# Kernel tuning notes

Measured on AMD Instinct MI355X. Metric: run time of the kernel, lower is better.

The kernel has to match this reference:

```python
import jax, jax.numpy as jnp
import numpy as np

B, S, D, H = 1, 4096, 1024, 16
DH = D // H

def setup_inputs() -> dict:
    key = jax.random.key(0)
    ks = jax.random.split(key, 5)
    std = float(np.sqrt(2.0 / (D + D)))
    return {
        "x": jax.random.normal(ks[0], (B, S, D), dtype=jnp.float32),
        "Wq": jax.random.normal(ks[1], (D, D), dtype=jnp.float32) * std,
        "Wk": jax.random.normal(ks[2], (D, D), dtype=jnp.float32) * std,
        "Wv": jax.random.normal(ks[3], (D, D), dtype=jnp.float32) * std,
        "Wo": jax.random.normal(ks[4], (D, D), dtype=jnp.float32) * std,
    }

def reference(x, Wq, Wk, Wv, Wo):
    # projections: input @ W.T, then split heads: b s (h d) -> b h s d
    def split_heads(t):
        b, s, _ = t.shape
        return t.reshape(b, s, H, DH).transpose(0, 2, 1, 3)
    q = split_heads(x @ Wq.T)
    k = split_heads(x @ Wk.T)
    v = split_heads(x @ Wv.T)
    scale = 1.0 / jnp.sqrt(jnp.asarray(DH, dtype=x.dtype))
    scores = jnp.einsum("bhqd,bhkd->bhqk", q, k) * scale  # (b,h,s,s)
    # causal mask: allow k <= q
    causal = jnp.tril(jnp.ones((S, S), dtype=bool))
    scores = jnp.where(causal, scores, jnp.finfo(scores.dtype).min)
    attn = jax.nn.softmax(scores, axis=-1)
    out = jnp.einsum("bhqk,bhkd->bhqd", attn, v)  # (b,h,s,d)
    out = out.transpose(0, 2, 1, 3).reshape(B, S, D)  # b h s d -> b s (h d)
    return out @ Wo.T
```

## Files before the change

### kernel.cpp

```cpp
#include <hip/hip_runtime.h>
#include <math.h>

#define SEQ 4096
#define DM  1024
#define NH  16
#define DH  64
#define NS  4

typedef _Float16 h16;
typedef __attribute__((ext_vector_type(4))) _Float16 h16x4;
typedef __attribute__((ext_vector_type(8))) _Float16 h16x8;
typedef __attribute__((ext_vector_type(4))) float f32x4;

__device__ __forceinline__ void gload_lds16(const h16* g, h16* l) {
    __builtin_amdgcn_global_load_lds(
        (const __attribute__((address_space(1))) void*)g,
        (__attribute__((address_space(3))) void*)l, 16, 0, 0);
}

__global__ __launch_bounds__(256) void cvt_all(const float* __restrict__ x,
                                               const float* __restrict__ wq,
                                               const float* __restrict__ wk,
                                               const float* __restrict__ wv,
                                               const float* __restrict__ wo,
                                               h16* __restrict__ dst) {
    const size_t SD4 = (size_t)SEQ * DM / 4;
    const size_t DD4 = (size_t)DM * DM / 4;
    const size_t i = (size_t)blockIdx.x * 256 + threadIdx.x;
    const float* src;
    size_t off;
    if (i < SD4) { src = x; off = i; }
    else {
        const size_t j = i - SD4;
        const int wsel = (int)(j >> 18);
        off = j & (DD4 - 1);
        src = (wsel == 0) ? wq : (wsel == 1) ? wk : (wsel == 2) ? wv : wo;
    }
    const float4 v = ((const float4*)src)[off];
    h16x4 o = { (h16)v.x, (h16)v.y, (h16)v.z, (h16)v.w };
    ((h16x4*)dst)[i] = o;
}

#define GT 32

__global__ __launch_bounds__(256) void gemm_qkv(const h16* __restrict__ xh,
                                                const h16* __restrict__ Wq,
                                                const h16* __restrict__ Wk,
                                                const h16* __restrict__ Wv,
                                                h16* __restrict__ Qh,
                                                h16* __restrict__ Kh,
                                                h16* __restrict__ Vth,
                                                float scl) {
    __shared__ h16 As[2][128 * GT];
    __shared__ h16 Bs[2][128 * GT];

    const int z    = blockIdx.z;
    const h16* B   = (z == 0) ? Wq : (z == 1) ? Wk : Wv;
    const int t    = threadIdx.x;
    const int lane = t & 63;
    const int w    = t >> 6;
    const int wm   = (w >> 1) * 64;
    const int wn   = (w & 1) * 64;
    const int l15  = lane & 15;
    const int lq   = lane >> 4;
    const int lq8  = lq * 8;
    const int m0   = blockIdx.y * 128;
    const int n0   = blockIdx.x * 128;
    const int K = DM, M = SEQ, N = DM;

    const int srow = w * 16 + (lane >> 2);
    const int scol = (lane & 3) * 8;
    const h16* pa0 = xh + (size_t)(m0 + srow) * K + scol;
    const h16* pa1 = xh + (size_t)(m0 + 64 + srow) * K + scol;
    const h16* pb0 = B  + (size_t)(n0 + srow) * K + scol;
    const h16* pb1 = B  + (size_t)(n0 + 64 + srow) * K + scol;

    f32x4 acc[4][4] = {};

    for (int k0 = 0; k0 < K; k0 += 64) {
        __syncthreads();
        #pragma unroll
        for (int s = 0; s < 2; ++s) {
            const int ko = k0 + s * 32;
            gload_lds16(pa0 + ko, &As[s][w * 512]);
            gload_lds16(pa1 + ko, &As[s][2048 + w * 512]);
            gload_lds16(pb0 + ko, &Bs[s][w * 512]);
            gload_lds16(pb1 + ko, &Bs[s][2048 + w * 512]);
        }
        __syncthreads();

        #pragma unroll
        for (int s = 0; s < 2; ++s) {
            h16x8 af[4], bf[4];
            #pragma unroll
            for (int i = 0; i < 4; ++i)
                af[i] = *(const h16x8*)&As[s][(wm + i * 16 + l15) * GT + lq8];
            #pragma unroll
            for (int j = 0; j < 4; ++j)
                bf[j] = *(const h16x8*)&Bs[s][(wn + j * 16 + l15) * GT + lq8];
            #pragma unroll
            for (int i = 0; i < 4; ++i)
                #pragma unroll
                for (int j = 0; j < 4; ++j)
                    acc[i][j] = __builtin_amdgcn_mfma_f32_16x16x32_f16(af[i], bf[j], acc[i][j], 0, 0, 0);
        }
    }

    const int cr = wm + lq * 4;
    const int cc = wn + l15;
    if (z == 2) {
        #pragma unroll
        for (int i = 0; i < 4; ++i)
            #pragma unroll
            for (int j = 0; j < 4; ++j) {
                const int gm0 = m0 + cr + i * 16;
                const int gn  = n0 + cc + j * 16;
                h16x4 v = { (h16)acc[i][j][0], (h16)acc[i][j][1],
                            (h16)acc[i][j][2], (h16)acc[i][j][3] };
                *(h16x4*)(Vth + (size_t)gn * M + gm0) = v;
            }
    } else {
        h16* Og = (z == 0) ? Qh : Kh;
        const float e = (z == 0) ? scl : 1.0f;
        #pragma unroll
        for (int i = 0; i < 4; ++i)
            #pragma unroll
            for (int j = 0; j < 4; ++j)
                #pragma unroll
                for (int r = 0; r < 4; ++r) {
                    const int gm = m0 + cr + i * 16 + r;
                    const int gn = n0 + cc + j * 16;
                    Og[(size_t)gm * N + gn] = (h16)(acc[i][j][r] * e);
                }
    }
}

__global__ __launch_bounds__(256) void gemm_out(const h16* __restrict__ A,
                                                const h16* __restrict__ B,
                                                float* __restrict__ C) {
    __shared__ h16 As[2][64 * GT];
    __shared__ h16 Bs[2][128 * GT];

    const int t    = threadIdx.x;
    const int lane = t & 63;
    const int w    = t >> 6;
    const int wm   = (w >> 1) * 32;
    const int wn   = (w & 1) * 64;
    const int l15  = lane & 15;
    const int lq   = lane >> 4;
    const int lq8  = lq * 8;
    const int m0   = blockIdx.y * 64;
    const int n0   = blockIdx.x * 128;
    const int K = DM, N = DM;

    const int srow = w * 16 + (lane >> 2);
    const int scol = (lane & 3) * 8;
    const h16* pa0 = A + (size_t)(m0 + srow) * K + scol;
    const h16* pb0 = B + (size_t)(n0 + srow) * K + scol;
    const h16* pb1 = B + (size_t)(n0 + 64 + srow) * K + scol;

    f32x4 acc[2][4] = {};

    for (int k0 = 0; k0 < K; k0 += 64) {
        __syncthreads();
        #pragma unroll
        for (int s = 0; s < 2; ++s) {
            const int ko = k0 + s * 32;
            gload_lds16(pa0 + ko, &As[s][w * 512]);
            gload_lds16(pb0 + ko, &Bs[s][w * 512]);
            gload_lds16(pb1 + ko, &Bs[s][2048 + w * 512]);
        }
        __syncthreads();

        #pragma unroll
        for (int s = 0; s < 2; ++s) {
            h16x8 af[2], bf[4];
            #pragma unroll
            for (int i = 0; i < 2; ++i)
                af[i] = *(const h16x8*)&As[s][(wm + i * 16 + l15) * GT + lq8];
            #pragma unroll
            for (int j = 0; j < 4; ++j)
                bf[j] = *(const h16x8*)&Bs[s][(wn + j * 16 + l15) * GT + lq8];
            #pragma unroll
            for (int i = 0; i < 2; ++i)
                #pragma unroll
                for (int j = 0; j < 4; ++j)
                    acc[i][j] = __builtin_amdgcn_mfma_f32_16x16x32_f16(af[i], bf[j], acc[i][j], 0, 0, 0);
        }
    }

    const int cr = wm + lq * 4;
    const int cc = wn + l15;
    #pragma unroll
    for (int i = 0; i < 2; ++i)
        #pragma unroll
        for (int j = 0; j < 4; ++j)
            #pragma unroll
            for (int r = 0; r < 4; ++r)
                C[(size_t)(m0 + cr + i * 16 + r) * N + n0 + cc + j * 16] = acc[i][j][r];
}

#define AST 80

__global__ __launch_bounds__(256, 3) void flash_attn_split(
        const h16* __restrict__ Qg, const h16* __restrict__ Kg,
        const h16* __restrict__ Vt, h16* __restrict__ OP,
        float* __restrict__ Mb, float* __restrict__ Lb) {
    __shared__ h16 Ks[64 * AST];
    __shared__ h16 Vs[64 * AST];
    __shared__ h16 Ps[64 * AST];

    const int qt   = 63 - (int)blockIdx.y;
    const int hh   = blockIdx.x;
    const int sp   = blockIdx.z;
    const int t    = threadIdx.x;
    const int lane = t & 63;
    const int w    = t >> 6;
    const int l15  = lane & 15;
    const int lq   = lane >> 4;
    const int lq8  = lq * 8;
    const int hc   = hh * DH;
    const int q0   = qt * 64;
    const int q_loc = w * 16 + l15;

    const int ntile = qt + 1;
    const int chunk = (ntile + NS - 1) / NS;
    const int kts   = sp * chunk;
    const int kte   = (kts + chunk < ntile) ? (kts + chunk) : ntile;

    const int r1 = t >> 3;
    const int r2 = r1 + 32;
    const int c1 = (t & 7) * 8;

    *(h16x8*)&Ks[r1 * AST + c1] = *(const h16x8*)(Qg + (size_t)(q0 + r1) * DM + hc + c1);
    *(h16x8*)&Ks[r2 * AST + c1] = *(const h16x8*)(Qg + (size_t)(q0 + r2) * DM + hc + c1);

    const int kb0 = kts * 64;
    h16x8 kv1 = *(const h16x8*)(Kg + (size_t)(kb0 + r1) * DM + hc + c1);
    h16x8 kv2 = *(const h16x8*)(Kg + (size_t)(kb0 + r2) * DM + hc + c1);
    h16x8 vv1 = *(const h16x8*)(Vt + (size_t)(hc + r1) * SEQ + kb0 + c1);
    h16x8 vv2 = *(const h16x8*)(Vt + (size_t)(hc + r2) * SEQ + kb0 + c1);

    __syncthreads();
    h16x8 qf[2];
    qf[0] = *(const h16x8*)&Ks[q_loc * AST + lq8];
    qf[1] = *(const h16x8*)&Ks[q_loc * AST + 32 + lq8];

    float m_st = -1e30f, l_st = 0.0f;
    f32x4 o[4] = {};
    h16* const ps = &Ps[(size_t)q_loc * AST];

    for (int kt = kts; kt < kte; ++kt) {
        __syncthreads();
        *(h16x8*)&Ks[r1 * AST + c1] = kv1;
        *(h16x8*)&Ks[r2 * AST + c1] = kv2;
        *(h16x8*)&Vs[r1 * AST + c1] = vv1;
        *(h16x8*)&Vs[r2 * AST + c1] = vv2;
        __syncthreads();
        if (kt + 1 < kte) {
            const int k0n = (kt + 1) * 64;
            kv1 = *(const h16x8*)(Kg + (size_t)(k0n + r1) * DM + hc + c1);
            kv2 = *(const h16x8*)(Kg + (size_t)(k0n + r2) * DM + hc + c1);
            vv1 = *(const h16x8*)(Vt + (size_t)(hc + r1) * SEQ + k0n + c1);
            vv2 = *(const h16x8*)(Vt + (size_t)(hc + r2) * SEQ + k0n + c1);
        }

        f32x4 s[4] = {};
        #pragma unroll
        for (int kc = 0; kc < 2; ++kc)
            #pragma unroll
            for (int jj = 0; jj < 4; ++jj) {
                const h16x8 kf = *(const h16x8*)&Ks[(jj * 16 + l15) * AST + kc * 32 + lq8];
                s[jj] = __builtin_amdgcn_mfma_f32_16x16x32_f16(kf, qf[kc], s[jj], 0, 0, 0);
            }

        if (kt == qt) {
            #pragma unroll
            for (int jj = 0; jj < 4; ++jj)
                #pragma unroll
                for (int r = 0; r < 4; ++r)
                    if ((jj * 16 + lq * 4 + r) > q_loc) s[jj][r] = -1e30f;
        }
        float mx = m_st;
        #pragma unroll
        for (int jj = 0; jj < 4; ++jj)
            #pragma unroll
            for (int r = 0; r < 4; ++r)
                mx = fmaxf(mx, s[jj][r]);
        mx = fmaxf(mx, __shfl_xor(mx, 16, 64));
        mx = fmaxf(mx, __shfl_xor(mx, 32, 64));
        const float alpha = exp2f(m_st - mx);
        m_st = mx;
        float sum = 0.0f;
        #pragma unroll
        for (int jj = 0; jj < 4; ++jj) {
            const float p0 = exp2f(s[jj][0] - mx);
            const float p1 = exp2f(s[jj][1] - mx);
            const float p2 = exp2f(s[jj][2] - mx);
            const float p3 = exp2f(s[jj][3] - mx);
            sum += (p0 + p1) + (p2 + p3);
            h16x4 pk = { (h16)p0, (h16)p1, (h16)p2, (h16)p3 };
            *(h16x4*)(ps + jj * 16 + lq * 4) = pk;
        }
        sum += __shfl_xor(sum, 16, 64);
        sum += __shfl_xor(sum, 32, 64);
        l_st = l_st * alpha + sum;
        #pragma unroll
        for (int jj = 0; jj < 4; ++jj)
            #pragma unroll
            for (int r = 0; r < 4; ++r)
                o[jj][r] *= alpha;

        asm volatile("s_waitcnt lgkmcnt(0)" ::: "memory");
        h16x8 pf[2];
        pf[0] = *(const h16x8*)(ps + lq8);
        pf[1] = *(const h16x8*)(ps + 32 + lq8);

        #pragma unroll
        for (int kc = 0; kc < 2; ++kc)
            #pragma unroll
            for (int jj = 0; jj < 4; ++jj) {
                const h16x8 vf = *(const h16x8*)&Vs[(jj * 16 + l15) * AST + kc * 32 + lq8];
                o[jj] = __builtin_amdgcn_mfma_f32_16x16x32_f16(vf, pf[kc], o[jj], 0, 0, 0);
            }
    }

    h16* const op = OP + (size_t)sp * SEQ * DM;
    const size_t qg = (size_t)(q0 + q_loc) * DM + hc;
    #pragma unroll
    for (int jj = 0; jj < 4; ++jj) {
        h16x4 ov = { (h16)o[jj][0], (h16)o[jj][1], (h16)o[jj][2], (h16)o[jj][3] };
        *(h16x4*)(op + qg + jj * 16 + lq * 4) = ov;
    }
    if (lq == 0) {
        const size_t mi = ((size_t)sp * NH + hh) * SEQ + q0 + q_loc;
        Mb[mi] = m_st;
        Lb[mi] = l_st;
    }
}

__global__ __launch_bounds__(256) void combine(const h16* __restrict__ OP,
                                               const float* __restrict__ Mb,
                                               const float* __restrict__ Lb,
                                               h16* __restrict__ AOh) {
    const int i  = blockIdx.x * 256 + threadIdx.x;
    const int q  = i >> 8;
    const int c4 = (i & 255) * 4;
    const int hh = c4 >> 6;

    float ms[NS], ls[NS];
    float mstar = -1e30f;
    #pragma unroll
    for (int s = 0; s < NS; ++s) {
        const size_t mi = ((size_t)s * NH + hh) * SEQ + q;
        ms[s] = Mb[mi];
        ls[s] = Lb[mi];
        mstar = fmaxf(mstar, ms[s]);
    }
    float L = 0.0f;
    float acc[4] = {};
    #pragma unroll
    for (int s = 0; s < NS; ++s) {
        const float ws = exp2f(ms[s] - mstar);
        L += ls[s] * ws;
        const h16x4 ov = *(const h16x4*)(OP + (size_t)s * SEQ * DM + (size_t)q * DM + c4);
        acc[0] += ws * (float)ov[0];
        acc[1] += ws * (float)ov[1];
        acc[2] += ws * (float)ov[2];
        acc[3] += ws * (float)ov[3];
    }
    const float inv = 1.0f / L;
    h16x4 r = { (h16)(acc[0] * inv), (h16)(acc[1] * inv),
                (h16)(acc[2] * inv), (h16)(acc[3] * inv) };
    *(h16x4*)(AOh + (size_t)q * DM + c4) = r;
}

extern "C" void kernel_launch(void* const* d_in, const int* in_sizes, int n_in,
                              void* d_out, int out_size, void* d_ws, size_t ws_size,
                              hipStream_t stream) {
    const float* x  = (const float*)d_in[0];
    const float* Wq = (const float*)d_in[1];
    const float* Wk = (const float*)d_in[2];
    const float* Wv = (const float*)d_in[3];
    const float* Wo = (const float*)d_in[4];
    float* out = (float*)d_out;

    const size_t SD = (size_t)SEQ * DM;
    const size_t DD = (size_t)DM * DM;

    h16* xh  = (h16*)d_ws;
    h16* wqh = xh + SD;
    h16* wkh = wqh + DD;
    h16* wvh = wkh + DD;
    h16* woh = wvh + DD;
    h16* Qh  = woh + DD;
    h16* Kh  = Qh + SD;
    h16* Vth = Kh + SD;
    h16* AOh = Vth + SD;
    h16* OP  = AOh + SD;
    float* Mb = (float*)(OP + (size_t)NS * SD);
    float* Lb = Mb + (size_t)NS * NH * SEQ;

    const dim3 blk(256);

    cvt_all<<<(int)((SD + 4 * DD) / 4 / 256), blk, 0, stream>>>(x, Wq, Wk, Wv, Wo, xh);

    const float SCL = 0.125f * 1.44269504088896340736f;

    gemm_qkv<<<dim3(DM / 128, SEQ / 128, 3), blk, 0, stream>>>(
        xh, wqh, wkh, wvh, Qh, Kh, Vth, SCL);

    flash_attn_split<<<dim3(NH, 64, NS), blk, 0, stream>>>(Qh, Kh, Vth, OP, Mb, Lb);

    combine<<<(int)(SD / 4 / 256), blk, 0, stream>>>(OP, Mb, Lb, AOh);

    gemm_out<<<dim3(DM / 128, SEQ / 64), blk, 0, stream>>>(AOh, woh, out);
}
```

Before: 221.8 us.

## Feed P from registers via 16x16x16 MFMA and use lazy max rescaling

The probability tile P is no longer written to LDS and read back. Instead the per-lane packed fp16 values feed 16x16x16 MFMAs directly, matching the score accumulator layout, and the Ps shared buffer is removed. The online softmax now rescales O and l only when the running max grows by more than a threshold of 5 (exp2 domain), and defers the cross-lane sum reduction to the end. Launch bounds raise the minimum blocks per CU from 3 to 6 to use the freed LDS. This trades the LDS round-trip and per-tile rescales for twice as many smaller MFMAs, and risks fp16 overflow headroom in P from the lazy max.

```diff
diff --git a/kernel.cpp b/kernel.cpp
--- a/kernel.cpp
+++ b/kernel.cpp
@@ -202,13 +202,12 @@
 
 #define AST 80
 
-__global__ __launch_bounds__(256, 3) void flash_attn_split(
+__global__ __launch_bounds__(256, 6) void flash_attn_split(
         const h16* __restrict__ Qg, const h16* __restrict__ Kg,
         const h16* __restrict__ Vt, h16* __restrict__ OP,
         float* __restrict__ Mb, float* __restrict__ Lb) {
     __shared__ h16 Ks[64 * AST];
     __shared__ h16 Vs[64 * AST];
-    __shared__ h16 Ps[64 * AST];
 
     const int qt   = 63 - (int)blockIdx.y;
     const int hh   = blockIdx.x;
@@ -248,7 +247,6 @@
 
     float m_st = -1e30f, l_st = 0.0f;
     f32x4 o[4] = {};
-    h16* const ps = &Ps[(size_t)q_loc * AST];
 
     for (int kt = kts; kt < kte; ++kt) {
         __syncthreads();
@@ -281,7 +279,7 @@
                 for (int r = 0; r < 4; ++r)
                     if ((jj * 16 + lq * 4 + r) > q_loc) s[jj][r] = -1e30f;
         }
-        float mx = m_st;
+        float mx = -1e30f;
         #pragma unroll
         for (int jj = 0; jj < 4; ++jj)
             #pragma unroll
@@ -289,47 +287,46 @@
                 mx = fmaxf(mx, s[jj][r]);
         mx = fmaxf(mx, __shfl_xor(mx, 16, 64));
         mx = fmaxf(mx, __shfl_xor(mx, 32, 64));
-        const float alpha = exp2f(m_st - mx);
-        m_st = mx;
-        float sum = 0.0f;
+        if (mx > m_st + 5.0f) {
+            const float alpha = exp2f(m_st - mx);
+            m_st = mx;
+            l_st *= alpha;
+            #pragma unroll
+            for (int jj = 0; jj < 4; ++jj)
+                #pragma unroll
+                for (int r = 0; r < 4; ++r)
+                    o[jj][r] *= alpha;
+        }
+
+        h16x4 pk[4];
         #pragma unroll
         for (int jj = 0; jj < 4; ++jj) {
-            const float p0 = exp2f(s[jj][0] - mx);
-            const float p1 = exp2f(s[jj][1] - mx);
-            const float p2 = exp2f(s[jj][2] - mx);
-            const float p3 = exp2f(s[jj][3] - mx);
-            sum += (p0 + p1) + (p2 + p3);
-            h16x4 pk = { (h16)p0, (h16)p1, (h16)p2, (h16)p3 };
-            *(h16x4*)(ps + jj * 16 + lq * 4) = pk;
-        }
-        sum += __shfl_xor(sum, 16, 64);
-        sum += __shfl_xor(sum, 32, 64);
-        l_st = l_st * alpha + sum;
-        #pragma unroll
-        for (int jj = 0; jj < 4; ++jj)
-            #pragma unroll
-            for (int r = 0; r < 4; ++r)
-                o[jj][r] *= alpha;
-
-        asm volatile("s_waitcnt lgkmcnt(0)" ::: "memory");
-        h16x8 pf[2];
-        pf[0] = *(const h16x8*)(ps + lq8);
-        pf[1] = *(const h16x8*)(ps + 32 + lq8);
-
-        #pragma unroll
-        for (int kc = 0; kc < 2; ++kc)
+            const float p0 = exp2f(s[jj][0] - m_st);
+            const float p1 = exp2f(s[jj][1] - m_st);
+            const float p2 = exp2f(s[jj][2] - m_st);
+            const float p3 = exp2f(s[jj][3] - m_st);
+            l_st += (p0 + p1) + (p2 + p3);
+            pk[jj] = h16x4{ (h16)p0, (h16)p1, (h16)p2, (h16)p3 };
+        }
+
+        #pragma unroll
+        for (int dd = 0; dd < 4; ++dd)
             #pragma unroll
             for (int jj = 0; jj < 4; ++jj) {
-                const h16x8 vf = *(const h16x8*)&Vs[(jj * 16 + l15) * AST + kc * 32 + lq8];
-                o[jj] = __builtin_amdgcn_mfma_f32_16x16x32_f16(vf, pf[kc], o[jj], 0, 0, 0);
+                const h16x4 vf = *(const h16x4*)&Vs[(dd * 16 + l15) * AST + jj * 16 + lq * 4];
+                o[dd] = __builtin_amdgcn_mfma_f32_16x16x16f16(vf, pk[jj], o[dd], 0, 0, 0);
             }
     }
+
+    l_st += __shfl_xor(l_st, 16, 64);
+    l_st += __shfl_xor(l_st, 32, 64);
 
     h16* const op = OP + (size_t)sp * SEQ * DM;
     const size_t qg = (size_t)(q0 + q_loc) * DM + hc;
     #pragma unroll
     for (int jj = 0; jj < 4; ++jj) {
-        h16x4 ov = { (h16)o[jj][0], (h16)o[jj][1], (h16)o[jj][2], (h16)o[jj][3] };
+        h16x4 ov = { (h16)o[jj][0], (h16)o[jj][1],
+                     (h16)o[jj][2], (h16)o[jj][3] };
         *(h16x4*)(op + qg + jj * 16 + lq * 4) = ov;
     }
     if (lq == 0) {
```

New measurement: 245.1 us. 1.11x slower.
